# Optimization experiments

Measured on AMD Instinct MI355X. Metric: run time of the kernel, lower is better.

Reference implementation:

```python
import jax, jax.numpy as jnp
import numpy as np

N, D, K = 65536, 4096, 16
LN_EPS = 1e-5
SN_EPS = 1e-12
MIN_NORM = 1e-15


def setup_inputs() -> dict:
    key = jax.random.key(0)
    k1, k2, k3, k4 = jax.random.split(key, 4)
    return {
        "x": jax.random.normal(k1, (N, D), dtype=jnp.float32),
        "gamma": jnp.ones((D,), dtype=jnp.float32),
        "beta": jnp.zeros((D,), dtype=jnp.float32),
        "W": jax.random.normal(k2, (K, D), dtype=jnp.float32) * 0.02,
        "u": jax.random.normal(k3, (K,), dtype=jnp.float32),
        "log_scale": jnp.float32(-2.0),
    }


def _l2_normalize(v, eps=SN_EPS):
    return v / (jnp.linalg.norm(v) + eps)


def reference(x, gamma, beta, W, u, log_scale):
    # LayerNorm over last dim
    mean = jnp.mean(x, axis=-1, keepdims=True)
    var = jnp.mean(jnp.square(x - mean), axis=-1, keepdims=True)
    xn = (x - mean) * jax.lax.rsqrt(var + LN_EPS) * gamma + beta

    # spectral norm of W: one power iteration (torch spectral_norm forward)
    v = _l2_normalize(W.T @ u)           # [D]
    u_new = _l2_normalize(W @ v)         # [K]
    sigma = u_new @ (W @ v)              # scalar, top singular value estimate
    W_sn = W / sigma

    # linear (no bias) + learned scale
    vout = xn @ W_sn.T                   # [N, K]
    scale = jax.nn.sigmoid(log_scale) * 0.5
    vout = vout * scale

    # Poincare ball expmap0 with c=1: tanh(||v||) * v / ||v||
    vnorm = jnp.maximum(jnp.linalg.norm(vout, axis=-1, keepdims=True), MIN_NORM)
    return jnp.tanh(vnorm) * vout / vnorm
```

## Files before the change

kernel.cpp:

```cpp
#include <hip/hip_runtime.h>
#include <hip/hip_bf16.h>


#define ND 4096
#define NK 16
#define NROWS 65536

using f32x4  = __attribute__((ext_vector_type(4))) float;
using bf16x8 = __attribute__((ext_vector_type(8))) short;

#define GWB_OFF  0u
#define T_OFF    131072u
#define PART_OFF 147456u
#define SC_OFF   149568u

__device__ __forceinline__ unsigned short f2bf(float f) {
    union { __hip_bfloat16 h; unsigned short u; } cv;
    cv.h = __float2bfloat16(f);
    return cv.u;
}

__global__ __launch_bounds__(256) void prep_a(
    const float* __restrict__ W, const float* __restrict__ gamma,
    const float* __restrict__ beta, const float* __restrict__ u,
    float* __restrict__ ws_t, unsigned short* __restrict__ ws_gwb,
    float* __restrict__ ws_part)
{
    const int d = blockIdx.x * 256 + threadIdx.x;
    float uu[NK];
#pragma unroll
    for (int k = 0; k < NK; ++k) uu[k] = u[k];
    const float g = gamma[d], b = beta[d];
    float w[NK];
#pragma unroll
    for (int k = 0; k < NK; ++k) w[k] = W[k * ND + d];
    float t = 0.f;
#pragma unroll
    for (int k = 0; k < NK; ++k) t = fmaf(w[k], uu[k], t);
    ws_t[d] = t;

    const int s  = d >> 5;
    const int wq = d & 31;
    const int lc = (wq >> 2) & 3;
    const int j  = (wq & 3) | ((wq >> 4) << 2);
    const int base = s * 512 + lc * 128 + j;
#pragma unroll
    for (int k = 0; k < NK; ++k) ws_gwb[base + k * 8] = f2bf(g * w[k]);

    __shared__ float red[256][34];
    red[threadIdx.x][0] = t * t;
#pragma unroll
    for (int k = 0; k < NK; ++k) {
        red[threadIdx.x][1 + k]  = g * w[k];
        red[threadIdx.x][17 + k] = b * w[k];
    }
    __syncthreads();
    for (int off = 128; off > 0; off >>= 1) {
        if (threadIdx.x < off)
            for (int v = 0; v < 33; ++v)
                red[threadIdx.x][v] += red[threadIdx.x + off][v];
        __syncthreads();
    }
    if (threadIdx.x < 33) ws_part[blockIdx.x * 33 + threadIdx.x] = red[0][threadIdx.x];
}

__global__ __launch_bounds__(256) void prep_b(
    const float* __restrict__ W, const float* __restrict__ ws_t,
    const float* __restrict__ ws_part, const float* __restrict__ log_scale,
    float* __restrict__ sc)
{
    __shared__ float tot[33];
    __shared__ float red[256][17];
    const int tid = threadIdx.x;
    if (tid < 33) {
        float s = 0.f;
        for (int b = 0; b < 16; ++b) s += ws_part[b * 33 + tid];
        tot[tid] = s;
    }
    __syncthreads();
    const float inv_nt = 1.0f / (sqrtf(tot[0]) + 1e-12f);
    float sp[NK];
#pragma unroll
    for (int k = 0; k < NK; ++k) sp[k] = 0.f;
    for (int jj = 0; jj < 16; ++jj) {
        const int d = tid * 16 + jj;
        const float vd = ws_t[d] * inv_nt;
#pragma unroll
        for (int k = 0; k < NK; ++k) sp[k] = fmaf(W[k * ND + d], vd, sp[k]);
    }
#pragma unroll
    for (int k = 0; k < NK; ++k) red[tid][k] = sp[k];
    __syncthreads();
    for (int off = 128; off > 0; off >>= 1) {
        if (tid < off)
            for (int v = 0; v < NK; ++v) red[tid][v] += red[tid + off][v];
        __syncthreads();
    }
    if (tid == 0) {
        float ns2 = 0.f;
        for (int k = 0; k < NK; ++k) ns2 += red[0][k] * red[0][k];
        const float sigma = ns2 / (sqrtf(ns2) + 1e-12f);
        const float scale = 0.5f / (1.0f + expf(-log_scale[0]));
        sc[0] = scale / sigma;
        for (int k = 0; k < NK; ++k) { sc[1 + k] = tot[1 + k]; sc[17 + k] = tot[17 + k]; }
    }
}

__global__ __launch_bounds__(1024, 4) void hyp_main(
    const float* __restrict__ x, const unsigned short* __restrict__ gwb_g,
    const float* __restrict__ sc, float* __restrict__ out)
{
    __shared__ unsigned short gwb[ND * NK];

    const int lane = threadIdx.x & 63;
    const int wid  = threadIdx.x >> 6;
    const int tile = (blockIdx.x << 4) + wid;
    const int lr = lane & 15;
    const int lc = lane >> 4;

    const float* xp = x + (size_t)(tile * 16 + lr) * ND + lc * 4;
    const unsigned short* lp = gwb + lane * 8;

    f32x4 xa = *(const f32x4*)(xp);
    f32x4 xb = *(const f32x4*)(xp + 16);

    {
        const uint4* src = (const uint4*)gwb_g;
        uint4* dst = (uint4*)gwb;
#pragma unroll
        for (int i = 0; i < 8; ++i)
            dst[threadIdx.x + i * 1024] = src[threadIdx.x + i * 1024];
    }
    __syncthreads();

    const float coef = sc[0];
    const float gk = sc[1 + lr];
    const float bk = sc[17 + lr];

    f32x4 acc = {0.f, 0.f, 0.f, 0.f};
    float s1 = 0.f, s2 = 0.f;

#define PROCESS(XA, XB, SS) do {                                          \
        bf16x8 afrag;                                                     \
        afrag[0] = (short)f2bf(XA[0]); afrag[1] = (short)f2bf(XA[1]);     \
        afrag[2] = (short)f2bf(XA[2]); afrag[3] = (short)f2bf(XA[3]);     \
        afrag[4] = (short)f2bf(XB[0]); afrag[5] = (short)f2bf(XB[1]);     \
        afrag[6] = (short)f2bf(XB[2]); afrag[7] = (short)f2bf(XB[3]);     \
        s1 += ((XA[0] + XA[1]) + (XA[2] + XA[3]))                         \
            + ((XB[0] + XB[1]) + (XB[2] + XB[3]));                        \
        s2 = fmaf(XA[0], XA[0], s2); s2 = fmaf(XA[1], XA[1], s2);         \
        s2 = fmaf(XA[2], XA[2], s2); s2 = fmaf(XA[3], XA[3], s2);         \
        s2 = fmaf(XB[0], XB[0], s2); s2 = fmaf(XB[1], XB[1], s2);         \
        s2 = fmaf(XB[2], XB[2], s2); s2 = fmaf(XB[3], XB[3], s2);         \
        bf16x8 bfrag = *(const bf16x8*)(lp + (SS) * 512);                 \
        acc = __builtin_amdgcn_mfma_f32_16x16x32_bf16(afrag, bfrag, acc, 0, 0, 0); \
    } while (0)

#pragma unroll 4
    for (int s = 0; s < 127; ++s) {
        f32x4 na = *(const f32x4*)(xp + (s + 1) * 32);
        f32x4 nb = *(const f32x4*)(xp + (s + 1) * 32 + 16);
        PROCESS(xa, xb, s);
        xa = na; xb = nb;
    }
    PROCESS(xa, xb, 127);
#undef PROCESS

    s1 += __shfl_xor(s1, 16); s1 += __shfl_xor(s1, 32);
    s2 += __shfl_xor(s2, 16); s2 += __shfl_xor(s2, 32);
    const float mean = s1 * (1.0f / ND);
    const float var  = s2 * (1.0f / ND) - mean * mean;
    const float rstd = rsqrtf(var + 1e-5f);

    float vout[4];
#pragma unroll
    for (int j = 0; j < 4; ++j) {
        const int r = lc * 4 + j;
        const float m_r  = __shfl(mean, r);
        const float rs_r = __shfl(rstd, r);
        vout[j] = coef * (fmaf(-m_r, gk, acc[j]) * rs_r + bk);
    }

    float nsq[4];
#pragma unroll
    for (int j = 0; j < 4; ++j) nsq[j] = vout[j] * vout[j];
#pragma unroll
    for (int m = 1; m < 16; m <<= 1) {
#pragma unroll
        for (int j = 0; j < 4; ++j) nsq[j] += __shfl_xor(nsq[j], m);
    }

#pragma unroll
    for (int j = 0; j < 4; ++j) {
        float nv = sqrtf(nsq[j]);
        nv = fmaxf(nv, 1e-15f);
        const float fac = tanhf(nv) / nv;
        out[(size_t)(tile * 16 + lc * 4 + j) * NK + lr] = vout[j] * fac;
    }
}

extern "C" void kernel_launch(void* const* d_in, const int* in_sizes, int n_in,
                              void* d_out, int out_size, void* d_ws, size_t ws_size,
                              hipStream_t stream) {
    const float* x     = (const float*)d_in[0];
    const float* gamma = (const float*)d_in[1];
    const float* beta  = (const float*)d_in[2];
    const float* W     = (const float*)d_in[3];
    const float* u     = (const float*)d_in[4];
    const float* ls    = (const float*)d_in[5];

    char* ws = (char*)d_ws;
    unsigned short* ws_gwb = (unsigned short*)(ws + GWB_OFF);
    float* ws_t    = (float*)(ws + T_OFF);
    float* ws_part = (float*)(ws + PART_OFF);
    float* sc      = (float*)(ws + SC_OFF);
    float* out     = (float*)d_out;

    prep_a<<<16, 256, 0, stream>>>(W, gamma, beta, u, ws_t, ws_gwb, ws_part);
    prep_b<<<1, 256, 0, stream>>>(W, ws_t, ws_part, ls, sc);
    hyp_main<<<256, 1024, 0, stream>>>(x, ws_gwb, sc, out);
}
```

Baseline: 214.7 us.

## Fold spectral-norm second pass into prep via W·t partials and stagger row-chunk order

```diff
diff --git a/kernel.cpp b/kernel.cpp
--- a/kernel.cpp
+++ b/kernel.cpp
@@ -10,9 +10,7 @@
 using bf16x8 = __attribute__((ext_vector_type(8))) short;
 
 #define GWB_OFF  0u
-#define T_OFF    131072u
-#define PART_OFF 147456u
-#define SC_OFF   149568u
+#define PART_OFF 131072u
 
 __device__ __forceinline__ unsigned short f2bf(float f) {
     union { __hip_bfloat16 h; unsigned short u; } cv;
@@ -20,13 +18,15 @@
     return cv.u;
 }
 
-__global__ __launch_bounds__(256) void prep_a(
+__global__ __launch_bounds__(256) void prep(
     const float* __restrict__ W, const float* __restrict__ gamma,
     const float* __restrict__ beta, const float* __restrict__ u,
-    float* __restrict__ ws_t, unsigned short* __restrict__ ws_gwb,
-    float* __restrict__ ws_part)
+    unsigned short* __restrict__ ws_gwb, float* __restrict__ ws_part)
 {
-    const int d = blockIdx.x * 256 + threadIdx.x;
+    const int tid = threadIdx.x;
+    const int d = blockIdx.x * 256 + tid;
+    const int lane = tid & 63, wid = tid >> 6;
+
     float uu[NK];
 #pragma unroll
     for (int k = 0; k < NK; ++k) uu[k] = u[k];
@@ -34,113 +34,97 @@
     float w[NK];
 #pragma unroll
     for (int k = 0; k < NK; ++k) w[k] = W[k * ND + d];
+
     float t = 0.f;
 #pragma unroll
     for (int k = 0; k < NK; ++k) t = fmaf(w[k], uu[k], t);
-    ws_t[d] = t;
 
     const int s  = d >> 5;
     const int wq = d & 31;
     const int lc = (wq >> 2) & 3;
     const int j  = (wq & 3) | ((wq >> 4) << 2);
     const int base = s * 512 + lc * 128 + j;
-#pragma unroll
-    for (int k = 0; k < NK; ++k) ws_gwb[base + k * 8] = f2bf(g * w[k]);
-
-    __shared__ float red[256][34];
-    red[threadIdx.x][0] = t * t;
+
+    float P[49];
 #pragma unroll
     for (int k = 0; k < NK; ++k) {
-        red[threadIdx.x][1 + k]  = g * w[k];
-        red[threadIdx.x][17 + k] = b * w[k];
+        const float gw = g * w[k];
+        ws_gwb[base + k * 8] = f2bf(gw);
+        P[k]      = gw;
+        P[16 + k] = b * w[k];
+        P[32 + k] = w[k] * t;
+    }
+    P[48] = t * t;
+
+#pragma unroll
+    for (int m = 1; m < 64; m <<= 1) {
+#pragma unroll
+        for (int v = 0; v < 49; ++v) P[v] += __shfl_xor(P[v], m);
+    }
+    __shared__ float wred[4][49];
+    if (lane == 0) {
+#pragma unroll
+        for (int v = 0; v < 49; ++v) wred[wid][v] = P[v];
     }
     __syncthreads();
-    for (int off = 128; off > 0; off >>= 1) {
-        if (threadIdx.x < off)
-            for (int v = 0; v < 33; ++v)
-                red[threadIdx.x][v] += red[threadIdx.x + off][v];
-        __syncthreads();
-    }
-    if (threadIdx.x < 33) ws_part[blockIdx.x * 33 + threadIdx.x] = red[0][threadIdx.x];
-}
-
-__global__ __launch_bounds__(256) void prep_b(
-    const float* __restrict__ W, const float* __restrict__ ws_t,
-    const float* __restrict__ ws_part, const float* __restrict__ log_scale,
-    float* __restrict__ sc)
-{
-    __shared__ float tot[33];
-    __shared__ float red[256][17];
-    const int tid = threadIdx.x;
-    if (tid < 33) {
-        float s = 0.f;
-        for (int b = 0; b < 16; ++b) s += ws_part[b * 33 + tid];
-        tot[tid] = s;
-    }
-    __syncthreads();
-    const float inv_nt = 1.0f / (sqrtf(tot[0]) + 1e-12f);
-    float sp[NK];
-#pragma unroll
-    for (int k = 0; k < NK; ++k) sp[k] = 0.f;
-    for (int jj = 0; jj < 16; ++jj) {
-        const int d = tid * 16 + jj;
-        const float vd = ws_t[d] * inv_nt;
-#pragma unroll
-        for (int k = 0; k < NK; ++k) sp[k] = fmaf(W[k * ND + d], vd, sp[k]);
-    }
-#pragma unroll
-    for (int k = 0; k < NK; ++k) red[tid][k] = sp[k];
-    __syncthreads();
-    for (int off = 128; off > 0; off >>= 1) {
-        if (tid < off)
-            for (int v = 0; v < NK; ++v) red[tid][v] += red[tid + off][v];
-        __syncthreads();
-    }
-    if (tid == 0) {
-        float ns2 = 0.f;
-        for (int k = 0; k < NK; ++k) ns2 += red[0][k] * red[0][k];
-        const float sigma = ns2 / (sqrtf(ns2) + 1e-12f);
-        const float scale = 0.5f / (1.0f + expf(-log_scale[0]));
-        sc[0] = scale / sigma;
-        for (int k = 0; k < NK; ++k) { sc[1 + k] = tot[1 + k]; sc[17 + k] = tot[17 + k]; }
-    }
+    if (tid < 49)
+        ws_part[blockIdx.x * 49 + tid] =
+            (wred[0][tid] + wred[1][tid]) + (wred[2][tid] + wred[3][tid]);
 }
 
 __global__ __launch_bounds__(1024, 4) void hyp_main(
     const float* __restrict__ x, const unsigned short* __restrict__ gwb_g,
-    const float* __restrict__ sc, float* __restrict__ out)
+    const float* __restrict__ ws_part, const float* __restrict__ log_scale,
+    float* __restrict__ out)
 {
     __shared__ unsigned short gwb[ND * NK];
-
-    const int lane = threadIdx.x & 63;
-    const int wid  = threadIdx.x >> 6;
+    __shared__ float scl[49];
+
+    const int tid  = threadIdx.x;
+    const int lane = tid & 63;
+    const int wid  = tid >> 6;
     const int tile = (blockIdx.x << 4) + wid;
     const int lr = lane & 15;
     const int lc = lane >> 4;
 
     const float* xp = x + (size_t)(tile * 16 + lr) * ND + lc * 4;
     const unsigned short* lp = gwb + lane * 8;
-
-    f32x4 xa = *(const f32x4*)(xp);
-    f32x4 xb = *(const f32x4*)(xp + 16);
+    const int start = (tile * 53) & 63;
+
+    const f32x4 xa0 = *(const f32x4*)(xp + start * 64);
+    const f32x4 xb0 = *(const f32x4*)(xp + start * 64 + 16);
+    const f32x4 xc0 = *(const f32x4*)(xp + start * 64 + 32);
+    const f32x4 xd0 = *(const f32x4*)(xp + start * 64 + 48);
 
     {
         const uint4* src = (const uint4*)gwb_g;
         uint4* dst = (uint4*)gwb;
 #pragma unroll
         for (int i = 0; i < 8; ++i)
-            dst[threadIdx.x + i * 1024] = src[threadIdx.x + i * 1024];
+            dst[tid + i * 1024] = src[tid + i * 1024];
+    }
+    if (tid < 49) {
+        float s = 0.f;
+#pragma unroll
+        for (int b = 0; b < 16; ++b) s += ws_part[b * 49 + tid];
+        scl[tid] = s;
     }
     __syncthreads();
 
-    const float coef = sc[0];
-    const float gk = sc[1 + lr];
-    const float bk = sc[17 + lr];
+    float ns2 = 0.f;
+#pragma unroll
+    for (int k = 0; k < NK; ++k) ns2 += scl[32 + k] * scl[32 + k];
+    const float nt   = sqrtf(scl[48]) + 1e-12f;
+    const float nwv  = sqrtf(ns2) / nt;
+    const float sigma = (nwv * nwv) / (nwv + 1e-12f);
+    const float coef = (0.5f / (1.0f + expf(-log_scale[0]))) / sigma;
+    const float gk = scl[lr];
+    const float bk = scl[16 + lr];
 
     f32x4 acc = {0.f, 0.f, 0.f, 0.f};
     float s1 = 0.f, s2 = 0.f;
 
-#define PROCESS(XA, XB, SS) do {                                          \
+#define HALF(XA, XB, SS) do {                                             \
         bf16x8 afrag;                                                     \
         afrag[0] = (short)f2bf(XA[0]); afrag[1] = (short)f2bf(XA[1]);     \
         afrag[2] = (short)f2bf(XA[2]); afrag[3] = (short)f2bf(XA[3]);     \
@@ -156,15 +140,27 @@
         acc = __builtin_amdgcn_mfma_f32_16x16x32_bf16(afrag, bfrag, acc, 0, 0, 0); \
     } while (0)
 
-#pragma unroll 4
-    for (int s = 0; s < 127; ++s) {
-        f32x4 na = *(const f32x4*)(xp + (s + 1) * 32);
-        f32x4 nb = *(const f32x4*)(xp + (s + 1) * 32 + 16);
-        PROCESS(xa, xb, s);
-        xa = na; xb = nb;
-    }
-    PROCESS(xa, xb, 127);
+#define PROCESS(II, XA, XB, XC, XD) do {                                  \
+        HALF(XA, XB, 2 * (II));                                           \
+        HALF(XC, XD, 2 * (II) + 1);                                       \
+    } while (0)
+
+#define LOADPROC(II) do {                                                 \
+        f32x4 xa = *(const f32x4*)(xp + (II) * 64);                       \
+        f32x4 xb = *(const f32x4*)(xp + (II) * 64 + 16);                  \
+        f32x4 xc = *(const f32x4*)(xp + (II) * 64 + 32);                  \
+        f32x4 xd = *(const f32x4*)(xp + (II) * 64 + 48);                  \
+        PROCESS(II, xa, xb, xc, xd);                                      \
+    } while (0)
+
+    PROCESS(start, xa0, xb0, xc0, xd0);
+#pragma unroll 2
+    for (int i = start + 1; i < 64; ++i) LOADPROC(i);
+#pragma unroll 2
+    for (int i = 0; i < start; ++i) LOADPROC(i);
+#undef LOADPROC
 #undef PROCESS
+#undef HALF
 
     s1 += __shfl_xor(s1, 16); s1 += __shfl_xor(s1, 32);
     s2 += __shfl_xor(s2, 16); s2 += __shfl_xor(s2, 32);
@@ -211,12 +207,9 @@
 
     char* ws = (char*)d_ws;
     unsigned short* ws_gwb = (unsigned short*)(ws + GWB_OFF);
-    float* ws_t    = (float*)(ws + T_OFF);
     float* ws_part = (float*)(ws + PART_OFF);
-    float* sc      = (float*)(ws + SC_OFF);
     float* out     = (float*)d_out;
 
-    prep_a<<<16, 256, 0, stream>>>(W, gamma, beta, u, ws_t, ws_gwb, ws_part);
-    prep_b<<<1, 256, 0, stream>>>(W, ws_t, ws_part, ls, sc);
-    hyp_main<<<256, 1024, 0, stream>>>(x, ws_gwb, sc, out);
-}
+    prep<<<16, 256, 0, stream>>>(W, gamma, beta, u, ws_gwb, ws_part);
+    hyp_main<<<256, 1024, 0, stream>>>(x, ws_gwb, ws_part, ls, out);
+}
```

Measured after the change: 199.7 us. 7.0% less time.
